# Kernel tuning notes

Hardware: AMD Instinct MI355X
Metric: run time of the kernel (lower is better)

Reference implementation:

```python
import jax, jax.numpy as jnp
import numpy as np

INPUT_DIM = 512
HIDDEN_DIM = 512


def setup_inputs() -> dict:
    key = jax.random.key(0)
    k1, k2 = jax.random.split(key, 2)
    T, B = 2048, 32
    x = jax.random.normal(k1, (T, B, INPUT_DIM), dtype=jnp.float32)
    hidden_state = jnp.zeros((1, B, HIDDEN_DIM), dtype=jnp.float32)
    cell_state = jnp.zeros((1, B, HIDDEN_DIM), dtype=jnp.float32)
    # xavier_uniform for weights, zeros for bias (matches init_weights)
    dim_size = INPUT_DIM + HIDDEN_DIM
    limit = np.sqrt(6.0 / (dim_size + 4 * HIDDEN_DIM)).astype(np.float32)
    weights = jax.random.uniform(k2, (dim_size, 4 * HIDDEN_DIM), dtype=jnp.float32,
                                 minval=-limit, maxval=limit)
    bias = jnp.zeros((4 * HIDDEN_DIM,), dtype=jnp.float32)
    return {"x": x, "hidden_state": hidden_state, "cell_state": cell_state,
            "weights": weights, "bias": bias}


def reference(x, hidden_state, cell_state, weights, bias):
    H = HIDDEN_DIM

    def step(carry, x_t):
        h, c = carry  # [1, B, H] each; x_t: [B, input_dim]
        concat = jnp.concatenate((x_t[None], h), axis=2)  # [1, B, in+H]
        gates = jnp.matmul(concat, weights) + bias        # [1, B, 4H]
        f = jax.nn.sigmoid(gates[:, :, :H])
        i = jax.nn.sigmoid(gates[:, :, H:2 * H])
        g = jnp.tanh(gates[:, :, 2 * H:3 * H])
        o = jax.nn.sigmoid(gates[:, :, 3 * H:])
        c_new = f * c + i * g
        h_new = o * jnp.tanh(c_new)
        return (h_new, c_new), h_new[0]  # emit [B, H]

    (h_f, c_f), outs = jax.lax.scan(step, (hidden_state, cell_state), x)
    return outs, (h_f, c_f)
```

## Files before the change

### kernel.cpp

```cpp
#include <hip/hip_runtime.h>
#include <math.h>

#define T_STEPS 2048
#define BATCH   32
#define IN_DIM  512
#define H_DIM   512
#define G4      2048
#define NWG     16
#define NTHR    512
#define GLS     132

typedef __attribute__((ext_vector_type(8))) short short8;
typedef __attribute__((ext_vector_type(4))) float f32x4;
typedef __attribute__((ext_vector_type(2))) float f32x2;
typedef __attribute__((ext_vector_type(4))) unsigned u32x4;

__device__ inline unsigned short f2bf(float f) {
    unsigned u = __builtin_bit_cast(unsigned, f);
    unsigned r = (u + 0x7FFFu + ((u >> 16) & 1u)) >> 16;
    return (unsigned short)r;
}
__device__ inline unsigned pack2(float a, float b) {
    return (unsigned)f2bf(a) | ((unsigned)f2bf(b) << 16);
}
__device__ inline float h2f(unsigned u) {
    _Float16 h = __builtin_bit_cast(_Float16, (unsigned short)(u & 0xFFFFu));
    return (float)h;
}
__device__ inline float fsigm(float x) {
    return __builtin_amdgcn_rcpf(1.f + __expf(-x));
}
__device__ inline float ftanh(float x) {
    return 1.f - 2.f * __builtin_amdgcn_rcpf(__expf(2.f * x) + 1.f);
}
__device__ inline float sigm(float v) { return 1.f / (1.f + expf(-v)); }

__device__ inline void ld4x_ic(const void* p0, const void* p1,
                               const void* p2, const void* p3,
                               u32x4& v0, u32x4& v1, u32x4& v2, u32x4& v3) {
    asm volatile(
        "global_load_dwordx4 %0, %4, off sc1\n\t"
        "global_load_dwordx4 %1, %5, off sc1\n\t"
        "global_load_dwordx4 %2, %6, off sc1\n\t"
        "global_load_dwordx4 %3, %7, off sc1\n\t"
        "s_waitcnt vmcnt(0)"
        : "=&v"(v0), "=&v"(v1), "=&v"(v2), "=&v"(v3)
        : "v"(p0), "v"(p1), "v"(p2), "v"(p3) : "memory");
}

__global__ __launch_bounds__(256) void wt_kernel(const float* __restrict__ W,
                                                 unsigned short* __restrict__ Wt) {
    __shared__ unsigned short tile[32][33];
    const int n0 = blockIdx.x << 5, k0 = blockIdx.y << 5;
    const int tx = threadIdx.x & 31, ty = threadIdx.x >> 5;
    #pragma unroll
    for (int r = 0; r < 32; r += 8)
        tile[ty + r][tx] = f2bf(W[(size_t)(k0 + ty + r) * G4 + n0 + tx]);
    __syncthreads();
    #pragma unroll
    for (int r = 0; r < 32; r += 8)
        Wt[(size_t)(n0 + ty + r) * 1024 + k0 + tx] = tile[tx][ty + r];
}

__global__ void init_h(const float* __restrict__ h0, unsigned short* __restrict__ hb) {
    int i = blockIdx.x * 256 + threadIdx.x;
    hb[i] = f2bf(h0[i]);
}

__global__ __launch_bounds__(256) void xw_mfma(const float* __restrict__ x,
                                               const unsigned short* __restrict__ Wt,
                                               const float* __restrict__ bias,
                                               _Float16* __restrict__ pre16) {
    __shared__ unsigned short As[64][40];
    __shared__ unsigned short Bs[64][40];
    const int tid = threadIdx.x;
    const int w = tid >> 6, l = tid & 63;
    const int m0 = blockIdx.y << 6, n0 = blockIdx.x << 6;
    const int srow = tid >> 2, sseg = (tid & 3) << 3;
    const int arow = (w << 4) + (l & 15);
    const int kb = (l >> 4) << 3;
    f32x4 acc[4] = {};

    for (int kc = 0; kc < 16; ++kc) {
        const float* xs = x + (size_t)(m0 + srow) * IN_DIM + kc * 32 + sseg;
        float4 xa = *(const float4*)xs;
        float4 xb2 = *(const float4*)(xs + 4);
        int4 av;
        av.x = pack2(xa.x, xa.y);  av.y = pack2(xa.z, xa.w);
        av.z = pack2(xb2.x, xb2.y); av.w = pack2(xb2.z, xb2.w);
        *(int4*)&As[srow][sseg] = av;
        *(int4*)&Bs[srow][sseg] = *(const int4*)(Wt + (size_t)(n0 + srow) * 1024 + kc * 32 + sseg);
        __syncthreads();
        short8 af = *(const short8*)&As[arow][kb];
        #pragma unroll
        for (int n = 0; n < 4; ++n) {
            short8 bf = *(const short8*)&Bs[(n << 4) + (l & 15)][kb];
            acc[n] = __builtin_amdgcn_mfma_f32_16x16x32_bf16(af, bf, acc[n], 0, 0, 0);
        }
        __syncthreads();
    }
    #pragma unroll
    for (int n = 0; n < 4; ++n) {
        const int col = n0 + (n << 4) + (l & 15);
        const float bb = bias[col];
        #pragma unroll
        for (int ri = 0; ri < 4; ++ri) {
            const int row = m0 + (w << 4) + ((l >> 4) << 2) + ri;
            pre16[(size_t)row * G4 + col] = (_Float16)(acc[n][ri] + bb);
        }
    }
}

__global__ __launch_bounds__(NTHR, 1) void lstm_scan(
        const unsigned short* __restrict__ Wt,
        const unsigned short* __restrict__ pre16u,
        const float* __restrict__ c0,
        unsigned short* __restrict__ hbuf,
        float* __restrict__ outs,
        float* __restrict__ hf, float* __restrict__ cf,
        unsigned int* __restrict__ flags) {
    __shared__ char Hl[32768];
    __shared__ float Gl[32 * GLS];

    const int g = blockIdx.x;
    const int tid = threadIdx.x;
    const int w = tid >> 6, l = tid & 63;

    const int gc = ((w >> 1) << 9) + (g << 5) + ((w & 1) << 4) + (l & 15);
    const int ksub = (l >> 4) << 3;
    short8 wfh[16];
    #pragma unroll
    for (int kc = 0; kc < 16; ++kc)
        wfh[kc] = *(const short8*)(Wt + (size_t)gc * 1024 + 512 + kc * 32 + ksub);

    const int b   = tid >> 4;
    const int hcp = (tid & 15) << 1;
    const int col = (g << 5) + hcp;
    float2 cv = *(const float2*)(c0 + (b << 9) + col);

    const int arow0 = l & 15, arow1 = (l & 15) + 16;
    const int kbyte = (l >> 4) << 4;
    const int swz0 = (arow0 & 7) << 4, swz1 = (arow1 & 7) << 4;
    const int lcw = (w << 4) + (l & 15);

    {
        const unsigned short* hp0 = hbuf + (w << 9) + (l << 3);
        u32x4 v0, v1, v2, v3;
        ld4x_ic(hp0, hp0 + 4096, hp0 + 8192, hp0 + 12288, v0, v1, v2, v3);
        char* hd = Hl + w * 1024 + ((l << 4) ^ (w << 4));
        *(u32x4*)hd = v0; *(u32x4*)(hd + 8192) = v1;
        *(u32x4*)(hd + 16384) = v2; *(u32x4*)(hd + 24576) = v3;
    }
    __syncthreads();

    unsigned puf, pui, pug, puo;
    {
        const unsigned* pp = (const unsigned*)(pre16u + ((size_t)b << 11) + col);
        asm volatile("global_load_dword %0, %4, off\n\t"
                     "global_load_dword %1, %4, off offset:1024\n\t"
                     "global_load_dword %2, %4, off offset:2048\n\t"
                     "global_load_dword %3, %4, off offset:3072"
                     : "=&v"(puf), "=&v"(pui), "=&v"(pug), "=&v"(puo)
                     : "v"(pp) : "memory");
    }

    for (int gt = 0; gt < T_STEPS; ++gt) {
        f32x4 acc0 = {0.f, 0.f, 0.f, 0.f}, acc1 = {0.f, 0.f, 0.f, 0.f};
        #pragma unroll
        for (int kc = 0; kc < 16; ++kc) {
            const int kb2 = kc * 64 + kbyte;
            short8 ha0 = *(const short8*)(Hl + arow0 * 1024 + (kb2 ^ swz0));
            short8 ha1 = *(const short8*)(Hl + arow1 * 1024 + (kb2 ^ swz1));
            acc0 = __builtin_amdgcn_mfma_f32_16x16x32_bf16(ha0, wfh[kc], acc0, 0, 0, 0);
            acc1 = __builtin_amdgcn_mfma_f32_16x16x32_bf16(ha1, wfh[kc], acc1, 0, 0, 0);
        }

        #pragma unroll
        for (int ri = 0; ri < 4; ++ri) {
            const int br = ((l >> 4) << 2) + ri;
            Gl[br * GLS + lcw] = acc0[ri];
            Gl[(br + 16) * GLS + lcw] = acc1[ri];
        }
        __syncthreads();

        asm volatile("s_waitcnt vmcnt(0)" ::: "memory");
        __builtin_amdgcn_sched_barrier(0);

        const float* grow = Gl + b * GLS + hcp;
        const float2 g_f = *(const float2*)(grow);
        const float2 g_i = *(const float2*)(grow + 32);
        const float2 g_g = *(const float2*)(grow + 64);
        const float2 g_o = *(const float2*)(grow + 96);
        const float f0 = fsigm(g_f.x + h2f(puf)), f1 = fsigm(g_f.y + h2f(puf >> 16));
        const float i0 = fsigm(g_i.x + h2f(pui)), i1 = fsigm(g_i.y + h2f(pui >> 16));
        const float g0 = ftanh(g_g.x + h2f(pug)), g1 = ftanh(g_g.y + h2f(pug >> 16));
        const float o0 = fsigm(g_o.x + h2f(puo)), o1 = fsigm(g_o.y + h2f(puo >> 16));
        cv.x = f0 * cv.x + i0 * g0;
        cv.y = f1 * cv.y + i1 * g1;
        const float hn0 = o0 * ftanh(cv.x);
        const float hn1 = o1 * ftanh(cv.y);

        {
            unsigned* hdst = (unsigned*)hbuf + (((gt + 1) & 1) << 13) + (b << 8) + (col >> 1);
            const unsigned pk = pack2(hn0, hn1);
            asm volatile("global_store_dword %0, %1, off sc1" :: "v"(hdst), "v"(pk) : "memory");
            float* optr = outs + ((size_t)gt << 14) + (b << 9) + col;
            f32x2 ov; ov.x = hn0; ov.y = hn1;
            asm volatile("global_store_dwordx2 %0, %1, off" :: "v"(optr), "v"(ov) : "memory");
        }
        if (gt == T_STEPS - 1) {
            *(float2*)(hf + (b << 9) + col) = make_float2(hn0, hn1);
            *(float2*)(cf + (b << 9) + col) = make_float2(cv.x, cv.y);
            break;
        }

        {
            const unsigned* pp = (const unsigned*)
                (pre16u + (((size_t)(gt + 1) << 5) + b) * 2048 + col);
            asm volatile("global_load_dword %0, %4, off\n\t"
                         "global_load_dword %1, %4, off offset:1024\n\t"
                         "global_load_dword %2, %4, off offset:2048\n\t"
                         "global_load_dword %3, %4, off offset:3072"
                         : "=&v"(puf), "=&v"(pui), "=&v"(pug), "=&v"(puo)
                         : "v"(pp) : "memory");
        }
        asm volatile("s_waitcnt vmcnt(5)" ::: "memory");

        __syncthreads();
        if (tid == 0)
            atomicAdd(flags + (g << 4), 1u);
        if (tid < 16) {
            unsigned* slot = flags + (tid << 4);
            const unsigned tgt = (unsigned)(gt + 1);
            for (;;) {
                unsigned vb;
                asm volatile("global_load_dword %0, %1, off sc1\n\ts_waitcnt vmcnt(0)"
                             : "=v"(vb) : "v"(slot) : "memory");
                if (vb >= tgt) break;
            }
        }
        __syncthreads();

        {
            const unsigned short* hsrc = hbuf + (((gt + 1) & 1) << 14) + (w << 9) + (l << 3);
            u32x4 v0, v1, v2, v3;
            ld4x_ic(hsrc, hsrc + 4096, hsrc + 8192, hsrc + 12288, v0, v1, v2, v3);
            char* hd = Hl + w * 1024 + ((l << 4) ^ (w << 4));
            *(u32x4*)hd = v0; *(u32x4*)(hd + 8192) = v1;
            *(u32x4*)(hd + 16384) = v2; *(u32x4*)(hd + 24576) = v3;
        }
        __syncthreads();
    }
}

__global__ __launch_bounds__(256) void lstm_step(const float* __restrict__ x_t,
                                                 const float* __restrict__ h_prev,
                                                 const float* __restrict__ W,
                                                 const float* __restrict__ bias,
                                                 const float* __restrict__ c_in,
                                                 float* __restrict__ c_out,
                                                 float* __restrict__ h_out,
                                                 float* __restrict__ hf,
                                                 float* __restrict__ cf, int last) {
    const int tid = threadIdx.x;
    const int hcc = tid & 7, b = tid >> 3;
    const int col = blockIdx.x * 8 + hcc;
    float a0 = bias[col], a1 = bias[col + 512], a2 = bias[col + 1024], a3 = bias[col + 1536];
    const float* xr = x_t + (size_t)b * IN_DIM;
    const float* hr = h_prev + (size_t)b * H_DIM;
    for (int k = 0; k < IN_DIM; ++k) {
        const float v = xr[k];
        const float* wk = &W[(size_t)k * G4 + col];
        a0 += v * wk[0]; a1 += v * wk[512]; a2 += v * wk[1024]; a3 += v * wk[1536];
    }
    for (int k = 0; k < H_DIM; ++k) {
        const float v = hr[k];
        const float* wk = &W[(size_t)(512 + k) * G4 + col];
        a0 += v * wk[0]; a1 += v * wk[512]; a2 += v * wk[1024]; a3 += v * wk[1536];
    }
    const float cn = sigm(a0) * c_in[(size_t)b * H_DIM + col] + sigm(a1) * tanhf(a2);
    const float hn = sigm(a3) * tanhf(cn);
    c_out[(size_t)b * H_DIM + col] = cn;
    h_out[(size_t)b * H_DIM + col] = hn;
    if (last) { hf[(size_t)b * H_DIM + col] = hn; cf[(size_t)b * H_DIM + col] = cn; }
}

extern "C" void kernel_launch(void* const* d_in, const int* in_sizes, int n_in,
                              void* d_out, int out_size, void* d_ws, size_t ws_size,
                              hipStream_t stream) {
    const float* x    = (const float*)d_in[0];
    const float* h0   = (const float*)d_in[1];
    const float* c0   = (const float*)d_in[2];
    const float* W    = (const float*)d_in[3];
    const float* bias = (const float*)d_in[4];

    float* outs = (float*)d_out;
    float* hf   = outs + (size_t)T_STEPS * BATCH * H_DIM;
    float* cf   = hf + BATCH * H_DIM;

    const size_t OFF_WT = 268435456ull;
    const size_t OFF_HB = OFF_WT + 4194304ull;
    const size_t OFF_FL = OFF_HB + 65536ull;
    const size_t NEED   = OFF_FL + 4096ull;

    if (ws_size >= NEED) {
        _Float16* pre16     = (_Float16*)d_ws;
        unsigned short* Wt  = (unsigned short*)((char*)d_ws + OFF_WT);
        unsigned short* hb  = (unsigned short*)((char*)d_ws + OFF_HB);
        unsigned int* flags = (unsigned int*)((char*)d_ws + OFF_FL);

        hipMemsetAsync(flags, 0, 4096, stream);
        wt_kernel<<<dim3(64, 32), 256, 0, stream>>>(W, Wt);
        init_h<<<64, 256, 0, stream>>>(h0, hb);
        xw_mfma<<<dim3(32, 1024), 256, 0, stream>>>(x, Wt, bias, pre16);
        lstm_scan<<<NWG, NTHR, 0, stream>>>(Wt, (const unsigned short*)pre16,
                                            c0, hb, outs, hf, cf, flags);
    } else {
        float* c_ws = (float*)d_ws;
        for (int t = 0; t < T_STEPS; ++t) {
            const float* hp = t ? outs + (size_t)(t - 1) * BATCH * H_DIM : h0;
            const float* ci = t ? c_ws : c0;
            lstm_step<<<64, 256, 0, stream>>>(x + (size_t)t * BATCH * IN_DIM,
                                              hp, W, bias, ci, c_ws,
                                              outs + (size_t)t * BATCH * H_DIM,
                                              hf, cf, (t == T_STEPS - 1) ? 1 : 0);
        }
    }
}
```

Measured before the change: 7.363 ms.

## Fuse input GEMM into the recurrent scan kernel with chunk-level producer/consumer flags

Merges the x·W input-projection GEMM and the sequential LSTM scan into one launch. 16 blocks run the recurrence while 512 extra blocks compute the pre-activations in time-ordered 64-step chunks and publish per-chunk counters, which the scan blocks poll before consuming each chunk. This lets the serial recurrence start while most of the GEMM is still running, and it drops one kernel launch. The step barrier is also reworked so every wave polls the flags itself instead of relying on an extra __syncthreads. The cost is a dependence on all 528 blocks being co-resident, since spin-waiting could deadlock otherwise. GEMM blocks may also contend with the scan blocks for memory bandwidth.

```diff
diff --git a/kernel.cpp b/kernel.cpp
--- a/kernel.cpp
+++ b/kernel.cpp
@@ -7,6 +7,7 @@
 #define H_DIM   512
 #define G4      2048
 #define NWG     16
+#define NXW     512
 #define NTHR    512
 #define GLS     132
 
@@ -67,64 +68,83 @@
     hb[i] = f2bf(h0[i]);
 }
 
-__global__ __launch_bounds__(256) void xw_mfma(const float* __restrict__ x,
-                                               const unsigned short* __restrict__ Wt,
-                                               const float* __restrict__ bias,
-                                               _Float16* __restrict__ pre16) {
-    __shared__ unsigned short As[64][40];
-    __shared__ unsigned short Bs[64][40];
-    const int tid = threadIdx.x;
-    const int w = tid >> 6, l = tid & 63;
-    const int m0 = blockIdx.y << 6, n0 = blockIdx.x << 6;
-    const int srow = tid >> 2, sseg = (tid & 3) << 3;
-    const int arow = (w << 4) + (l & 15);
-    const int kb = (l >> 4) << 3;
-    f32x4 acc[4] = {};
-
-    for (int kc = 0; kc < 16; ++kc) {
-        const float* xs = x + (size_t)(m0 + srow) * IN_DIM + kc * 32 + sseg;
-        float4 xa = *(const float4*)xs;
-        float4 xb2 = *(const float4*)(xs + 4);
-        int4 av;
-        av.x = pack2(xa.x, xa.y);  av.y = pack2(xa.z, xa.w);
-        av.z = pack2(xb2.x, xb2.y); av.w = pack2(xb2.z, xb2.w);
-        *(int4*)&As[srow][sseg] = av;
-        *(int4*)&Bs[srow][sseg] = *(const int4*)(Wt + (size_t)(n0 + srow) * 1024 + kc * 32 + sseg);
-        __syncthreads();
-        short8 af = *(const short8*)&As[arow][kb];
-        #pragma unroll
-        for (int n = 0; n < 4; ++n) {
-            short8 bf = *(const short8*)&Bs[(n << 4) + (l & 15)][kb];
-            acc[n] = __builtin_amdgcn_mfma_f32_16x16x32_bf16(af, bf, acc[n], 0, 0, 0);
-        }
-        __syncthreads();
-    }
-    #pragma unroll
-    for (int n = 0; n < 4; ++n) {
-        const int col = n0 + (n << 4) + (l & 15);
-        const float bb = bias[col];
-        #pragma unroll
-        for (int ri = 0; ri < 4; ++ri) {
-            const int row = m0 + (w << 4) + ((l >> 4) << 2) + ri;
-            pre16[(size_t)row * G4 + col] = (_Float16)(acc[n][ri] + bb);
-        }
-    }
-}
-
-__global__ __launch_bounds__(NTHR, 1) void lstm_scan(
+__global__ __launch_bounds__(NTHR, 1) void lstm_fused(
         const unsigned short* __restrict__ Wt,
-        const unsigned short* __restrict__ pre16u,
+        const float* __restrict__ x,
+        const float* __restrict__ bias,
+        unsigned short* __restrict__ pre16u,
         const float* __restrict__ c0,
         unsigned short* __restrict__ hbuf,
         float* __restrict__ outs,
         float* __restrict__ hf, float* __restrict__ cf,
-        unsigned int* __restrict__ flags) {
-    __shared__ char Hl[32768];
-    __shared__ float Gl[32 * GLS];
-
-    const int g = blockIdx.x;
+        unsigned* __restrict__ sync_area) {
+    __shared__ char LDS_[49664];
+    const int bid = blockIdx.x;
     const int tid = threadIdx.x;
+    unsigned* flags    = sync_area;
+    unsigned* chunkcnt = sync_area + 512;
+
+    if (bid >= NWG) {
+        const int xid  = bid - NWG;
+        const int half = tid >> 8;
+        const int t256 = tid & 255;
+        unsigned short (*As)[40] = (unsigned short(*)[40])(LDS_ + half * 10240);
+        unsigned short (*Bs)[40] = (unsigned short(*)[40])(LDS_ + half * 10240 + 5120);
+        const int ht  = xid * 2 + half;
+        const int bn  = ht & 31, bml = ht >> 5;
+        const int n0  = bn << 6;
+        const int w2  = t256 >> 6, l2 = t256 & 63;
+        const int srow = t256 >> 2, sseg = (t256 & 3) << 3;
+        const int arow = (w2 << 4) + (l2 & 15);
+        const int kb   = (l2 >> 4) << 3;
+
+        for (int iter = 0; iter < 32; ++iter) {
+            const int m0 = ((iter << 5) + bml) << 6;
+            f32x4 acc[4] = {};
+            for (int kc = 0; kc < 16; ++kc) {
+                const float* xs = x + (size_t)(m0 + srow) * IN_DIM + kc * 32 + sseg;
+                float4 xa = *(const float4*)xs;
+                float4 xb2 = *(const float4*)(xs + 4);
+                int4 av;
+                av.x = pack2(xa.x, xa.y);  av.y = pack2(xa.z, xa.w);
+                av.z = pack2(xb2.x, xb2.y); av.w = pack2(xb2.z, xb2.w);
+                *(int4*)&As[srow][sseg] = av;
+                *(int4*)&Bs[srow][sseg] =
+                    *(const int4*)(Wt + (size_t)(n0 + srow) * 1024 + kc * 32 + sseg);
+                __syncthreads();
+                short8 af = *(const short8*)&As[arow][kb];
+                #pragma unroll
+                for (int n = 0; n < 4; ++n) {
+                    short8 bf = *(const short8*)&Bs[(n << 4) + (l2 & 15)][kb];
+                    acc[n] = __builtin_amdgcn_mfma_f32_16x16x32_bf16(af, bf, acc[n], 0, 0, 0);
+                }
+                __syncthreads();
+            }
+            #pragma unroll
+            for (int n = 0; n < 4; ++n) {
+                const int col = n0 + (n << 4) + (l2 & 15);
+                const float bb = bias[col];
+                #pragma unroll
+                for (int ri = 0; ri < 4; ++ri) {
+                    const int row = m0 + (w2 << 4) + ((l2 >> 4) << 2) + ri;
+                    const _Float16 hv = (_Float16)(acc[n][ri] + bb);
+                    const unsigned hv32 = (unsigned)__builtin_bit_cast(unsigned short, hv);
+                    unsigned short* pd = pre16u + (size_t)row * G4 + col;
+                    asm volatile("global_store_short %0, %1, off sc1"
+                                 :: "v"(pd), "v"(hv32) : "memory");
+                }
+            }
+            asm volatile("s_waitcnt vmcnt(0)" ::: "memory");
+            __syncthreads();
+            if (tid == 0) atomicAdd(chunkcnt + iter, 2u);
+        }
+        return;
+    }
+
+    const int g = bid;
     const int w = tid >> 6, l = tid & 63;
+    char* Hl = LDS_;
+    float* Gl = (float*)(LDS_ + 32768);
 
     const int gc = ((w >> 1) << 9) + (g << 5) + ((w & 1) << 4) + (l & 15);
     const int ksub = (l >> 4) << 3;
@@ -153,13 +173,20 @@
     }
     __syncthreads();
 
+    for (;;) {
+        unsigned vb;
+        asm volatile("global_load_dword %0, %1, off sc1\n\ts_waitcnt vmcnt(0)"
+                     : "=v"(vb) : "v"(chunkcnt) : "memory");
+        if (vb >= 1024u) break;
+        __builtin_amdgcn_s_sleep(4);
+    }
     unsigned puf, pui, pug, puo;
     {
         const unsigned* pp = (const unsigned*)(pre16u + ((size_t)b << 11) + col);
-        asm volatile("global_load_dword %0, %4, off\n\t"
-                     "global_load_dword %1, %4, off offset:1024\n\t"
-                     "global_load_dword %2, %4, off offset:2048\n\t"
-                     "global_load_dword %3, %4, off offset:3072"
+        asm volatile("global_load_dword %0, %4, off sc1\n\t"
+                     "global_load_dword %1, %4, off offset:1024 sc1\n\t"
+                     "global_load_dword %2, %4, off offset:2048 sc1\n\t"
+                     "global_load_dword %3, %4, off offset:3072 sc1"
                      : "=&v"(puf), "=&v"(pui), "=&v"(pug), "=&v"(puo)
                      : "v"(pp) : "memory");
     }
@@ -214,13 +241,24 @@
             break;
         }
 
+        if (((gt + 1) & 63) == 0) {
+            const unsigned* cc = chunkcnt + ((gt + 1) >> 6);
+            for (;;) {
+                unsigned vb;
+                asm volatile("global_load_dword %0, %1, off sc1\n\ts_waitcnt vmcnt(0)"
+                             : "=v"(vb) : "v"(cc) : "memory");
+                if (vb >= 1024u) break;
+                __builtin_amdgcn_s_sleep(2);
+            }
+        }
+
         {
             const unsigned* pp = (const unsigned*)
                 (pre16u + (((size_t)(gt + 1) << 5) + b) * 2048 + col);
-            asm volatile("global_load_dword %0, %4, off\n\t"
-                         "global_load_dword %1, %4, off offset:1024\n\t"
-                         "global_load_dword %2, %4, off offset:2048\n\t"
-                         "global_load_dword %3, %4, off offset:3072"
+            asm volatile("global_load_dword %0, %4, off sc1\n\t"
+                         "global_load_dword %1, %4, off offset:1024 sc1\n\t"
+                         "global_load_dword %2, %4, off offset:2048 sc1\n\t"
+                         "global_load_dword %3, %4, off offset:3072 sc1"
                          : "=&v"(puf), "=&v"(pui), "=&v"(pug), "=&v"(puo)
                          : "v"(pp) : "memory");
         }
@@ -229,8 +267,9 @@
         __syncthreads();
         if (tid == 0)
             atomicAdd(flags + (g << 4), 1u);
-        if (tid < 16) {
-            unsigned* slot = flags + (tid << 4);
+
+        {
+            unsigned* slot = flags + ((l >> 2) << 4);
             const unsigned tgt = (unsigned)(gt + 1);
             for (;;) {
                 unsigned vb;
@@ -238,10 +277,6 @@
                              : "=v"(vb) : "v"(slot) : "memory");
                 if (vb >= tgt) break;
             }
-        }
-        __syncthreads();
-
-        {
             const unsigned short* hsrc = hbuf + (((gt + 1) & 1) << 14) + (w << 9) + (l << 3);
             u32x4 v0, v1, v2, v3;
             ld4x_ic(hsrc, hsrc + 4096, hsrc + 8192, hsrc + 12288, v0, v1, v2, v3);
@@ -300,21 +335,20 @@
 
     const size_t OFF_WT = 268435456ull;
     const size_t OFF_HB = OFF_WT + 4194304ull;
-    const size_t OFF_FL = OFF_HB + 65536ull;
-    const size_t NEED   = OFF_FL + 4096ull;
+    const size_t OFF_SY = OFF_HB + 65536ull;
+    const size_t NEED   = OFF_SY + 4096ull;
 
     if (ws_size >= NEED) {
-        _Float16* pre16     = (_Float16*)d_ws;
-        unsigned short* Wt  = (unsigned short*)((char*)d_ws + OFF_WT);
-        unsigned short* hb  = (unsigned short*)((char*)d_ws + OFF_HB);
-        unsigned int* flags = (unsigned int*)((char*)d_ws + OFF_FL);
-
-        hipMemsetAsync(flags, 0, 4096, stream);
+        unsigned short* pre16u = (unsigned short*)d_ws;
+        unsigned short* Wt     = (unsigned short*)((char*)d_ws + OFF_WT);
+        unsigned short* hb     = (unsigned short*)((char*)d_ws + OFF_HB);
+        unsigned* sync_a       = (unsigned*)((char*)d_ws + OFF_SY);
+
+        hipMemsetAsync(sync_a, 0, 4096, stream);
         wt_kernel<<<dim3(64, 32), 256, 0, stream>>>(W, Wt);
         init_h<<<64, 256, 0, stream>>>(h0, hb);
-        xw_mfma<<<dim3(32, 1024), 256, 0, stream>>>(x, Wt, bias, pre16);
-        lstm_scan<<<NWG, NTHR, 0, stream>>>(Wt, (const unsigned short*)pre16,
-                                            c0, hb, outs, hf, cf, flags);
+        lstm_fused<<<NWG + NXW, NTHR, 0, stream>>>(Wt, x, bias, pre16u, c0, hb,
+                                                   outs, hf, cf, sync_a);
     } else {
         float* c_ws = (float*)d_ws;
         for (int t = 0; t < T_STEPS; ++t) {
```

Result: slower. 8.149 ms (+10.7%).
